# Optimization experiments

Measured on AMD Instinct MI355X. Metric: run time of the kernel, lower is better.

## Reference

```python
import jax, jax.numpy as jnp
import numpy as np

B, L, C, H = 8, 1024, 1024, 16  # batch, seq_len, n_embed, n_head


def setup_inputs() -> dict:
    key = jax.random.key(0)
    k0, k1, k2 = jax.random.split(key, 3)
    s = 0.02  # init scale
    return {
        "x": jax.random.normal(k0, (B, L, C), jnp.float32),
        "W_qkv": jax.random.normal(k1, (C, 3 * C), jnp.float32) * s,  # (in, out) layout
        "b_qkv": jnp.zeros((3 * C,), jnp.float32),
        "W_proj": jax.random.normal(k2, (C, C), jnp.float32) * s,
        "b_proj": jnp.zeros((C,), jnp.float32),
    }


def reference(x, W_qkv, b_qkv, W_proj, b_proj):
    Bb, Ll, Cc = x.shape
    d = Cc // H  # head dim
    qkv = x @ W_qkv + b_qkv                      # (B, L, 3C)
    q, k, v = jnp.split(qkv, 3, axis=2)
    q = q.reshape(Bb, Ll, H, d).transpose(0, 2, 1, 3)  # (B, H, L, d)
    k = k.reshape(Bb, Ll, H, d).transpose(0, 2, 1, 3)
    v = v.reshape(Bb, Ll, H, d).transpose(0, 2, 1, 3)
    scale = 1.0 / np.sqrt(d).astype(np.float32)
    attn = jnp.einsum("bhid,bhjd->bhij", q, k) * scale  # (B, H, Lq, Lk)
    causal = jnp.tril(jnp.ones((Ll, Ll), dtype=bool))    # (Lq, Lk)
    attn = jnp.where(causal[None, None, :, :], attn, -jnp.inf)
    # NOTE: source uses F.softmax(attn, dim=2) -> softmax over the QUERY axis.
    attn = jax.nn.softmax(attn, axis=2)
    y = jnp.einsum("bhij,bhjd->bhid", attn, v)           # (B, H, L, d)
    y = y.transpose(0, 2, 1, 3).reshape(Bb, Ll, Cc)      # (B, L, C)
    return y @ W_proj + b_proj
```

## Files before the change

kernel.cpp:

```cpp
#include <hip/hip_runtime.h>

typedef unsigned short u16;
typedef unsigned int   u32;
using bf16x8 = __attribute__((ext_vector_type(8))) short;
using f32x4  = __attribute__((ext_vector_type(4))) float;
using f32x16 = __attribute__((ext_vector_type(16))) float;
using u32x4  = __attribute__((ext_vector_type(4))) u32;

static constexpr int Bb = 8, Ll = 1024, Cc = 1024, Hh = 16, Dd = 64;
static constexpr int Mrows = Bb * Ll;
static constexpr int N3    = 3 * Cc;
static constexpr float QSCALE = 0.125f * 1.44269504088896f;

__device__ __forceinline__ u16 f2b(float f) {
    u32 u = __builtin_bit_cast(u32, f);
    u += 0x7FFFu + ((u >> 16) & 1u);
    return (u16)(u >> 16);
}
__device__ __forceinline__ float b2f(u16 u) {
    return __builtin_bit_cast(float, (u32)u << 16);
}
__device__ __forceinline__ u32 pack2bf(float a, float b) {
    return (u32)f2b(a) | ((u32)f2b(b) << 16);
}
__device__ __forceinline__ void gload16(const u16* g, u16* l) {
    __builtin_amdgcn_global_load_lds(
        (const __attribute__((address_space(1))) void*)g,
        (__attribute__((address_space(3))) void*)l, 16, 0, 0);
}

__global__ void k_f32_to_bf16(const float* __restrict__ in, u16* __restrict__ out, int n16) {
    int idx = blockIdx.x * blockDim.x + threadIdx.x;
    if (idx >= n16) return;
    #pragma unroll
    for (int h = 0; h < 2; ++h) {
        f32x4 v0 = *((const f32x4*)in + idx * 4 + h * 2);
        f32x4 v1 = *((const f32x4*)in + idx * 4 + h * 2 + 1);
        u32x4 o;
        o[0] = pack2bf(v0[0], v0[1]);
        o[1] = pack2bf(v0[2], v0[3]);
        o[2] = pack2bf(v1[0], v1[1]);
        o[3] = pack2bf(v1[2], v1[3]);
        *((u32x4*)out + idx * 2 + h) = o;
    }
}

__global__ void k_transpose_w(const float* __restrict__ Wqkv, u16* __restrict__ WqkvT,
                              const float* __restrict__ Wproj, u16* __restrict__ WprojT) {
    __shared__ float tile[32][33];
    int bx = blockIdx.x;
    const float* in; u16* out; int Cn;
    if (bx < 96) { in = Wqkv;  out = WqkvT;  Cn = N3; }
    else         { in = Wproj; out = WprojT; Cn = Cc; bx -= 96; }
    const int R = Cc;
    int tx = threadIdx.x, ty = threadIdx.y;
    int c = bx * 32 + tx;
    int rbase = blockIdx.y * 32;
    #pragma unroll
    for (int rr = 0; rr < 4; ++rr)
        tile[ty + rr * 8][tx] = in[(size_t)(rbase + ty + rr * 8) * Cn + c];
    __syncthreads();
    int ro = bx * 32 + ty;
    #pragma unroll
    for (int rr = 0; rr < 4; ++rr)
        out[(size_t)(ro + rr * 8) * R + rbase + tx] = f2b(tile[tx][ty + rr * 8]);
}

__global__ void k_transpose_scale_bf16(const u16* __restrict__ in, const float* __restrict__ zinv,
                                       u16* __restrict__ out, int R, int Cn) {
    __shared__ u16 tile[32][33];
    int bh = blockIdx.z;
    size_t base = (size_t)bh * R * Cn;
    int tx = threadIdx.x, ty = threadIdx.y;
    int c = blockIdx.x * 32 + tx;
    int rbase = blockIdx.y * 32;
    #pragma unroll
    for (int rr = 0; rr < 4; ++rr)
        tile[ty + rr * 8][tx] = in[base + (size_t)(rbase + ty + rr * 8) * Cn + c];
    __syncthreads();
    float zv = zinv[(size_t)bh * R + rbase + tx];
    int ro = blockIdx.x * 32 + ty;
    #pragma unroll
    for (int rr = 0; rr < 4; ++rr)
        out[base + (size_t)(ro + rr * 8) * R + rbase + tx] = f2b(b2f(tile[tx][ty + rr * 8]) * zv);
}

__global__ __launch_bounds__(256, 2)
void k_gemm_qkv32(const u16* __restrict__ A, const u16* __restrict__ Bt,
                  const float* __restrict__ bias,
                  u16* __restrict__ qo, u16* __restrict__ ko, u16* __restrict__ vo)
{
    const int K = Cc;
    const int NT = K / 64;
    __shared__ u16 As[2][128 * 64];
    __shared__ u16 Bs[2][128 * 64];
    const int tid = threadIdx.x;
    const int wid = tid >> 6, lane = tid & 63;
    const int l31 = lane & 31, lhi = lane >> 5, l7 = lane & 7;
    const int wr = wid >> 1, wc = wid & 1;
    const int nwg = gridDim.x * gridDim.y;
    const int flat = blockIdx.y * gridDim.x + blockIdx.x;
    const int swz = (flat & 7) * (nwg >> 3) + (flat >> 3);
    const int bx = swz % gridDim.x, by = swz / gridDim.x;
    const int row0 = by * 128, col0 = bx * 128;

    const int srow = tid >> 3;
    const int schunk = (tid & 7) ^ (srow & 7);
    const u16* gA = A  + (size_t)(row0 + srow) * K + schunk * 8;
    const u16* gB = Bt + (size_t)(col0 + srow) * K + schunk * 8;

#define STG(buf, t) do { \
    const u16* ga_ = gA + (size_t)(t) * 64; \
    const u16* gb_ = gB + (size_t)(t) * 64; \
    u16* la_ = &As[buf][wid * 512]; \
    u16* lb_ = &Bs[buf][wid * 512]; \
    gload16(ga_,                  la_); \
    gload16(ga_ + (size_t)32 * K, la_ + 2048); \
    gload16(ga_ + (size_t)64 * K, la_ + 4096); \
    gload16(ga_ + (size_t)96 * K, la_ + 6144); \
    gload16(gb_,                  lb_); \
    gload16(gb_ + (size_t)32 * K, lb_ + 2048); \
    gload16(gb_ + (size_t)64 * K, lb_ + 4096); \
    gload16(gb_ + (size_t)96 * K, lb_ + 6144); \
} while (0)

    const int coff0 = (((0 + lhi) ^ l7) << 3);
    const int coff1 = (((2 + lhi) ^ l7) << 3);
    const int coff2 = (((4 + lhi) ^ l7) << 3);
    const int coff3 = (((6 + lhi) ^ l7) << 3);
    const int coff[4] = { coff0, coff1, coff2, coff3 };

    f32x16 acc[2][2] = {};

    STG(0, 0);
    STG(1, 1);
    asm volatile("s_waitcnt vmcnt(8)" ::: "memory");
    __builtin_amdgcn_s_barrier();
    __builtin_amdgcn_sched_barrier(0);

    for (int t = 0; t < NT; ++t) {
        const u16* cA = &As[t & 1][0];
        const u16* cB = &Bs[t & 1][0];
        bf16x8 af[2][4], bf0[4];
        #pragma unroll
        for (int tm = 0; tm < 2; ++tm)
            #pragma unroll
            for (int kc = 0; kc < 4; ++kc)
                af[tm][kc] = *(const bf16x8*)&cA[(wr * 64 + tm * 32 + l31) * 64 + coff[kc]];
        #pragma unroll
        for (int kc = 0; kc < 4; ++kc)
            bf0[kc] = *(const bf16x8*)&cB[(wc * 64 + l31) * 64 + coff[kc]];
        __builtin_amdgcn_s_setprio(1);
        #pragma unroll
        for (int tm = 0; tm < 2; ++tm)
            #pragma unroll
            for (int kc = 0; kc < 4; ++kc)
                acc[tm][0] = __builtin_amdgcn_mfma_f32_32x32x16_bf16(
                    af[tm][kc], bf0[kc], acc[tm][0], 0, 0, 0);
        __builtin_amdgcn_s_setprio(0);
        __builtin_amdgcn_s_barrier();
        bf16x8 bf1[4];
        #pragma unroll
        for (int kc = 0; kc < 4; ++kc)
            bf1[kc] = *(const bf16x8*)&cB[(wc * 64 + 32 + l31) * 64 + coff[kc]];
        __builtin_amdgcn_s_setprio(1);
        #pragma unroll
        for (int tm = 0; tm < 2; ++tm)
            #pragma unroll
            for (int kc = 0; kc < 4; ++kc)
                acc[tm][1] = __builtin_amdgcn_mfma_f32_32x32x16_bf16(
                    af[tm][kc], bf1[kc], acc[tm][1], 0, 0, 0);
        __builtin_amdgcn_s_setprio(0);
        __builtin_amdgcn_s_barrier();
        __builtin_amdgcn_sched_barrier(0);
        if (t + 2 < NT) STG(t & 1, t + 2);
        if (t + 1 < NT) {
            if (t + 2 < NT) { asm volatile("s_waitcnt vmcnt(8)" ::: "memory"); }
            else            { asm volatile("s_waitcnt vmcnt(0)" ::: "memory"); }
            __builtin_amdgcn_s_barrier();
            __builtin_amdgcn_sched_barrier(0);
        }
    }
#undef STG

    #pragma unroll
    for (int tm = 0; tm < 2; ++tm) {
        #pragma unroll
        for (int tn = 0; tn < 2; ++tn) {
            int cg = col0 + wc * 64 + tn * 32 + l31;
            float bv = bias[cg];
            int which = cg >> 10;
            float sc = (which == 0) ? QSCALE : 1.0f;
            int cc2 = cg & 1023;
            int h = cc2 >> 6, dd = cc2 & 63;
            int rbase = row0 + wr * 64 + tm * 32 + 4 * lhi;
            #pragma unroll
            for (int g = 0; g < 4; ++g) {
                #pragma unroll
                for (int r = 0; r < 4; ++r) {
                    int rg = rbase + 8 * g + r;
                    int bidx = rg >> 10, ll2 = rg & 1023;
                    size_t o = ((size_t)(bidx * Hh + h) * Ll + ll2) * Dd + dd;
                    u16 val = f2b((acc[tm][tn][g * 4 + r] + bv) * sc);
                    if (which == 0) qo[o] = val;
                    else if (which == 1) ko[o] = val;
                    else vo[o] = val;
                }
            }
        }
    }
}

__global__ __launch_bounds__(256, 2)
void k_gemm_proj32(const u16* __restrict__ A, const u16* __restrict__ Bt,
                   const float* __restrict__ bias, float* __restrict__ outf)
{
    const int K = Cc;
    const int N = Cc;
    const int NT = K / 64;
    __shared__ u16 As[2][128 * 64];
    __shared__ u16 Bs[2][128 * 64];
    const int tid = threadIdx.x;
    const int wid = tid >> 6, lane = tid & 63;
    const int l31 = lane & 31, lhi = lane >> 5, l7 = lane & 7;
    const int wr = wid >> 1, wc = wid & 1;
    const int nwg = gridDim.x * gridDim.y;
    const int flat = blockIdx.y * gridDim.x + blockIdx.x;
    const int swz = (flat & 7) * (nwg >> 3) + (flat >> 3);
    const int bx = swz % gridDim.x, by = swz / gridDim.x;
    const int row0 = by * 128, col0 = bx * 128;

    const int srow = tid >> 3;
    const int schunk = (tid & 7) ^ (srow & 7);
    const u16* gA = A  + (size_t)(row0 + srow) * K + schunk * 8;
    const u16* gB = Bt + (size_t)(col0 + srow) * K + schunk * 8;

#define STG(buf, t) do { \
    const u16* ga_ = gA + (size_t)(t) * 64; \
    const u16* gb_ = gB + (size_t)(t) * 64; \
    u16* la_ = &As[buf][wid * 512]; \
    u16* lb_ = &Bs[buf][wid * 512]; \
    gload16(ga_,                  la_); \
    gload16(ga_ + (size_t)32 * K, la_ + 2048); \
    gload16(ga_ + (size_t)64 * K, la_ + 4096); \
    gload16(ga_ + (size_t)96 * K, la_ + 6144); \
    gload16(gb_,                  lb_); \
    gload16(gb_ + (size_t)32 * K, lb_ + 2048); \
    gload16(gb_ + (size_t)64 * K, lb_ + 4096); \
    gload16(gb_ + (size_t)96 * K, lb_ + 6144); \
} while (0)

    const int coff0 = (((0 + lhi) ^ l7) << 3);
    const int coff1 = (((2 + lhi) ^ l7) << 3);
    const int coff2 = (((4 + lhi) ^ l7) << 3);
    const int coff3 = (((6 + lhi) ^ l7) << 3);
    const int coff[4] = { coff0, coff1, coff2, coff3 };

    f32x16 acc[2][2] = {};

    STG(0, 0);
    STG(1, 1);
    asm volatile("s_waitcnt vmcnt(8)" ::: "memory");
    __builtin_amdgcn_s_barrier();
    __builtin_amdgcn_sched_barrier(0);

    for (int t = 0; t < NT; ++t) {
        const u16* cA = &As[t & 1][0];
        const u16* cB = &Bs[t & 1][0];
        bf16x8 af[2][4], bf0[4];
        #pragma unroll
        for (int tm = 0; tm < 2; ++tm)
            #pragma unroll
            for (int kc = 0; kc < 4; ++kc)
                af[tm][kc] = *(const bf16x8*)&cA[(wr * 64 + tm * 32 + l31) * 64 + coff[kc]];
        #pragma unroll
        for (int kc = 0; kc < 4; ++kc)
            bf0[kc] = *(const bf16x8*)&cB[(wc * 64 + l31) * 64 + coff[kc]];
        __builtin_amdgcn_s_setprio(1);
        #pragma unroll
        for (int tm = 0; tm < 2; ++tm)
            #pragma unroll
            for (int kc = 0; kc < 4; ++kc)
                acc[tm][0] = __builtin_amdgcn_mfma_f32_32x32x16_bf16(
                    af[tm][kc], bf0[kc], acc[tm][0], 0, 0, 0);
        __builtin_amdgcn_s_setprio(0);
        __builtin_amdgcn_s_barrier();
        bf16x8 bf1[4];
        #pragma unroll
        for (int kc = 0; kc < 4; ++kc)
            bf1[kc] = *(const bf16x8*)&cB[(wc * 64 + 32 + l31) * 64 + coff[kc]];
        __builtin_amdgcn_s_setprio(1);
        #pragma unroll
        for (int tm = 0; tm < 2; ++tm)
            #pragma unroll
            for (int kc = 0; kc < 4; ++kc)
                acc[tm][1] = __builtin_amdgcn_mfma_f32_32x32x16_bf16(
                    af[tm][kc], bf1[kc], acc[tm][1], 0, 0, 0);
        __builtin_amdgcn_s_setprio(0);
        __builtin_amdgcn_s_barrier();
        __builtin_amdgcn_sched_barrier(0);
        if (t + 2 < NT) STG(t & 1, t + 2);
        if (t + 1 < NT) {
            if (t + 2 < NT) { asm volatile("s_waitcnt vmcnt(8)" ::: "memory"); }
            else            { asm volatile("s_waitcnt vmcnt(0)" ::: "memory"); }
            __builtin_amdgcn_s_barrier();
            __builtin_amdgcn_sched_barrier(0);
        }
    }
#undef STG

    #pragma unroll
    for (int tm = 0; tm < 2; ++tm) {
        #pragma unroll
        for (int tn = 0; tn < 2; ++tn) {
            int cg = col0 + wc * 64 + tn * 32 + l31;
            float bv = bias[cg];
            int rbase = row0 + wr * 64 + tm * 32 + 4 * lhi;
            #pragma unroll
            for (int g = 0; g < 4; ++g) {
                #pragma unroll
                for (int r = 0; r < 4; ++r) {
                    int rg = rbase + 8 * g + r;
                    outf[(size_t)rg * N + cg] = acc[tm][tn][g * 4 + r] + bv;
                }
            }
        }
    }
}

__global__ __launch_bounds__(256, 4)
void k_attn_colsum(const u16* __restrict__ Q, const u16* __restrict__ Kb,
                   float* __restrict__ zinv)
{
    __shared__ u16 Qs[2][64 * 64];
    const int tid = threadIdx.x;
    const int wid = tid >> 6, lane = tid & 63;
    const int lr = lane & 15, lg = lane >> 4;
    const int l7 = lr & 7;
    const int fid = blockIdx.x;
    const int xcd = fid & 7, n = fid >> 3;
    const int xtA = n & 7;
    const int xtB = 15 - xtA;
    const int bh = (xcd << 4) | (n >> 3);
    const u16* Qp = Q  + (size_t)bh * Ll * Dd;
    const u16* Kp = Kb + (size_t)bh * Ll * Dd;
    const int jwA = xtA * 64 + wid * 16;
    const int jwB = xtB * 64 + wid * 16;
    bf16x8 kbA0 = *(const bf16x8*)&Kp[(jwA + lr) * Dd + lg * 8];
    bf16x8 kbA1 = *(const bf16x8*)&Kp[(jwA + lr) * Dd + 32 + lg * 8];
    bf16x8 kbB0 = *(const bf16x8*)&Kp[(jwB + lr) * Dd + lg * 8];
    bf16x8 kbB1 = *(const bf16x8*)&Kp[(jwB + lr) * Dd + 32 + lg * 8];
    const bool dmask[4] = { lg * 4 + 0 >= lr, lg * 4 + 1 >= lr,
                            lg * 4 + 2 >= lr, lg * 4 + 3 >= lr };
    const int ch0 = ((lg ^ l7) << 3);
    const int ch1 = (((4 + lg) ^ l7) << 3);
    const int srow = tid >> 3;
    const int schunk = (tid & 7) ^ (srow & 7);
    float zA = 0.f, zB = 0.f;

    const int nA = 16 - xtA;
    const int NS = 17;
#define IOF(s) (((s) < nA) ? (xtA * 64 + 64 * (s)) : (xtB * 64 + 64 * ((s) - nA)))

#define STGQ(buf, I0) do { \
    const u16* g_ = Qp + (size_t)((I0) + srow) * 64 + schunk * 8; \
    u16* l_ = &Qs[buf][wid * 512]; \
    gload16(g_,                   l_); \
    gload16(g_ + (size_t)32 * 64, l_ + 2048); \
} while (0)

#define CS_STEP(buf, I0, JW, KB0, KB1, ZACC) do { \
    const u16* Qs_ = &Qs[buf][0]; \
    _Pragma("unroll") \
    for (int ss = 0; ss < 4; ++ss) { \
        int ib = (I0) + ss * 16; \
        if (ib >= (JW)) { \
            bf16x8 qa0 = *(const bf16x8*)&Qs_[(ss * 16 + lr) * 64 + ch0]; \
            bf16x8 qa1 = *(const bf16x8*)&Qs_[(ss * 16 + lr) * 64 + ch1]; \
            f32x4 s_ = {0.f, 0.f, 0.f, 0.f}; \
            s_ = __builtin_amdgcn_mfma_f32_16x16x32_bf16(qa0, KB0, s_, 0, 0, 0); \
            s_ = __builtin_amdgcn_mfma_f32_16x16x32_bf16(qa1, KB1, s_, 0, 0, 0); \
            if (ib >= (JW) + 16) { \
                _Pragma("unroll") \
                for (int r = 0; r < 4; ++r) ZACC += exp2f(s_[r]); \
            } else { \
                _Pragma("unroll") \
                for (int r = 0; r < 4; ++r) ZACC += dmask[r] ? exp2f(s_[r]) : 0.f; \
            } \
        } \
    } \
} while (0)

    STGQ(0, IOF(0));
    STGQ(1, IOF(1));
    asm volatile("s_waitcnt vmcnt(2)" ::: "memory");
    __builtin_amdgcn_s_barrier();
    __builtin_amdgcn_sched_barrier(0);

    for (int s = 0; s < NS; ++s) {
        if (s < nA) { CS_STEP((s & 1), xtA * 64 + 64 * s, jwA, kbA0, kbA1, zA); }
        else        { CS_STEP((s & 1), xtB * 64 + 64 * (s - nA), jwB, kbB0, kbB1, zB); }
        __builtin_amdgcn_s_barrier();
        __builtin_amdgcn_sched_barrier(0);
        if (s + 2 < NS) STGQ((s & 1), IOF(s + 2));
        if (s + 1 < NS) {
            if (s + 2 < NS) { asm volatile("s_waitcnt vmcnt(2)" ::: "memory"); }
            else            { asm volatile("s_waitcnt vmcnt(0)" ::: "memory"); }
            __builtin_amdgcn_s_barrier();
            __builtin_amdgcn_sched_barrier(0);
        }
    }
#undef STGQ
#undef CS_STEP
#undef IOF

    zA += __shfl_xor(zA, 16); zA += __shfl_xor(zA, 32);
    zB += __shfl_xor(zB, 16); zB += __shfl_xor(zB, 32);
    if (lg == 0) {
        zinv[(size_t)bh * Ll + jwA + lr] = 1.f / zA;
        zinv[(size_t)bh * Ll + jwB + lr] = 1.f / zB;
    }
}

__global__ __launch_bounds__(256, 4)
void k_attn_pv(const u16* __restrict__ Q, const u16* __restrict__ Kb,
               const u16* __restrict__ Vt, u16* __restrict__ Y)
{
    __shared__ u16 Ks[2][64 * 64];
    __shared__ u16 Vs[2][64 * 64];
    const int tid = threadIdx.x;
    const int wid = tid >> 6, lane = tid & 63;
    const int lr = lane & 15, lg = lane >> 4;
    const int l7 = lr & 7;
    const int fid = blockIdx.x;
    const int xcd = fid & 7, n = fid >> 3;
    const int xtA = n & 7;
    const int xtB = 15 - xtA;
    const int bh = (xcd << 4) | (n >> 3);
    const int bidx = bh >> 4, h = bh & 15;
    const u16* Qp = Q  + (size_t)bh * Ll * Dd;
    const u16* Kp = Kb + (size_t)bh * Ll * Dd;
    const u16* Vp = Vt + (size_t)bh * Ll * Dd;
    const int src0 = lr + 32 * (lg & 1);
    const int src1 = src0 + 16;
    const bool selHi = (lg & 2) != 0;
    const int ch0 = ((lg ^ l7) << 3);
    const int ch1 = (((4 + lg) ^ l7) << 3);
    const int srow = tid >> 3;
    const int schunk = (tid & 7) ^ (srow & 7);

    const int iwA = xtA * 64 + wid * 16;
    const int iwB = xtB * 64 + wid * 16;
    bf16x8 qaA0 = *(const bf16x8*)&Qp[(iwA + lr) * Dd + lg * 8];
    bf16x8 qaA1 = *(const bf16x8*)&Qp[(iwA + lr) * Dd + 32 + lg * 8];
    bf16x8 qaB0 = *(const bf16x8*)&Qp[(iwB + lr) * Dd + lg * 8];
    bf16x8 qaB1 = *(const bf16x8*)&Qp[(iwB + lr) * Dd + 32 + lg * 8];
    f32x4 yaccA[4] = {};
    f32x4 yaccB[4] = {};

    const int NS = 17;
#define JOF(s) (((s) <= xtA) ? 64 * (s) : 64 * ((s) - xtA - 1))

#define STGKV(buf, J) do { \
    const u16* gk_ = Kp + (size_t)((J) + srow) * 64 + schunk * 8; \
    const u16* gv_ = Vp + (size_t)srow * Ll + (J) + schunk * 8; \
    u16* lk_ = &Ks[buf][wid * 512]; \
    u16* lv_ = &Vs[buf][wid * 512]; \
    gload16(gk_,                   lk_); \
    gload16(gk_ + (size_t)32 * 64, lk_ + 2048); \
    gload16(gv_,                   lv_); \
    gload16(gv_ + (size_t)32 * Ll, lv_ + 2048); \
} while (0)

#define PV_STEP(buf, J0, IW, QA0, QA1, YACC) do { \
    const u16* Ks_ = &Ks[buf][0]; \
    const u16* Vs_ = &Vs[buf][0]; \
    uint2 w0, w1, w2, w3; \
    _Pragma("unroll") \
    for (int cs = 0; cs < 4; ++cs) { \
        bf16x8 kb0 = *(const bf16x8*)&Ks_[(cs * 16 + lr) * 64 + ch0]; \
        bf16x8 kb1 = *(const bf16x8*)&Ks_[(cs * 16 + lr) * 64 + ch1]; \
        f32x4 s_ = {0.f, 0.f, 0.f, 0.f}; \
        s_ = __builtin_amdgcn_mfma_f32_16x16x32_bf16(kb0, QA0, s_, 0, 0, 0); \
        s_ = __builtin_amdgcn_mfma_f32_16x16x32_bf16(kb1, QA1, s_, 0, 0, 0); \
        int jb = (J0) + cs * 16; \
        float p[4]; \
        if (jb + 15 <= (IW)) { \
            _Pragma("unroll") \
            for (int r = 0; r < 4; ++r) p[r] = exp2f(s_[r]); \
        } else { \
            int ig = (IW) + lr; \
            _Pragma("unroll") \
            for (int r = 0; r < 4; ++r) \
                p[r] = (jb + 4 * lg + r <= ig) ? exp2f(s_[r]) : 0.f; \
        } \
        uint2 w_; \
        w_.x = pack2bf(p[0], p[1]); \
        w_.y = pack2bf(p[2], p[3]); \
        if (cs == 0) w0 = w_; else if (cs == 1) w1 = w_; \
        else if (cs == 2) w2 = w_; else w3 = w_; \
    } \
    u32 a00 = (u32)__shfl((int)w0.x, src0), a01 = (u32)__shfl((int)w0.y, src0); \
    u32 a02 = (u32)__shfl((int)w0.x, src1), a03 = (u32)__shfl((int)w0.y, src1); \
    u32 a10 = (u32)__shfl((int)w1.x, src0), a11 = (u32)__shfl((int)w1.y, src0); \
    u32 a12 = (u32)__shfl((int)w1.x, src1), a13 = (u32)__shfl((int)w1.y, src1); \
    u32 a20 = (u32)__shfl((int)w2.x, src0), a21 = (u32)__shfl((int)w2.y, src0); \
    u32 a22 = (u32)__shfl((int)w2.x, src1), a23 = (u32)__shfl((int)w2.y, src1); \
    u32 a30 = (u32)__shfl((int)w3.x, src0), a31 = (u32)__shfl((int)w3.y, src0); \
    u32 a32 = (u32)__shfl((int)w3.x, src1), a33 = (u32)__shfl((int)w3.y, src1); \
    u32x4 pa0u, pa1u; \
    pa0u[0] = selHi ? a10 : a00;  pa0u[1] = selHi ? a11 : a01; \
    pa0u[2] = selHi ? a12 : a02;  pa0u[3] = selHi ? a13 : a03; \
    pa1u[0] = selHi ? a30 : a20;  pa1u[1] = selHi ? a31 : a21; \
    pa1u[2] = selHi ? a32 : a22;  pa1u[3] = selHi ? a33 : a23; \
    bf16x8 pa0 = __builtin_bit_cast(bf16x8, pa0u); \
    bf16x8 pa1 = __builtin_bit_cast(bf16x8, pa1u); \
    _Pragma("unroll") \
    for (int ns = 0; ns < 4; ++ns) { \
        bf16x8 vb0 = *(const bf16x8*)&Vs_[(ns * 16 + lr) * 64 + ch0]; \
        bf16x8 vb1 = *(const bf16x8*)&Vs_[(ns * 16 + lr) * 64 + ch1]; \
        YACC[ns] = __builtin_amdgcn_mfma_f32_16x16x32_bf16(pa0, vb0, YACC[ns], 0, 0, 0); \
        YACC[ns] = __builtin_amdgcn_mfma_f32_16x16x32_bf16(pa1, vb1, YACC[ns], 0, 0, 0); \
    } \
} while (0)

    STGKV(0, 0);
    STGKV(1, JOF(1));
    asm volatile("s_waitcnt vmcnt(4)" ::: "memory");
    __builtin_amdgcn_s_barrier();
    __builtin_amdgcn_sched_barrier(0);

    for (int s = 0; s < NS; ++s) {
        if (s <= xtA) { PV_STEP((s & 1), 64 * s, iwA, qaA0, qaA1, yaccA); }
        else          { PV_STEP((s & 1), 64 * (s - xtA - 1), iwB, qaB0, qaB1, yaccB); }
        __builtin_amdgcn_s_barrier();
        __builtin_amdgcn_sched_barrier(0);
        if (s + 2 < NS) STGKV((s & 1), JOF(s + 2));
        if (s + 1 < NS) {
            if (s + 2 < NS) { asm volatile("s_waitcnt vmcnt(4)" ::: "memory"); }
            else            { asm volatile("s_waitcnt vmcnt(0)" ::: "memory"); }
            __builtin_amdgcn_s_barrier();
            __builtin_amdgcn_sched_barrier(0);
        }
    }
#undef STGKV
#undef PV_STEP
#undef JOF

    #pragma unroll
    for (int ns = 0; ns < 4; ++ns)
        #pragma unroll
        for (int r = 0; r < 4; ++r) {
            int l2 = iwA + lg * 4 + r;
            Y[((size_t)bidx * Ll + l2) * Cc + h * Dd + ns * 16 + lr] = f2b(yaccA[ns][r]);
        }
    #pragma unroll
    for (int ns = 0; ns < 4; ++ns)
        #pragma unroll
        for (int r = 0; r < 4; ++r) {
            int l2 = iwB + lg * 4 + r;
            Y[((size_t)bidx * Ll + l2) * Cc + h * Dd + ns * 16 + lr] = f2b(yaccB[ns][r]);
        }
}

extern "C" void kernel_launch(void* const* d_in, const int* in_sizes, int n_in,
                              void* d_out, int out_size, void* d_ws, size_t ws_size,
                              hipStream_t stream)
{
    const float* x     = (const float*)d_in[0];
    const float* Wqkv  = (const float*)d_in[1];
    const float* bqkv  = (const float*)d_in[2];
    const float* Wproj = (const float*)d_in[3];
    const float* bproj = (const float*)d_in[4];
    float* out = (float*)d_out;

    char* ws = (char*)d_ws;
    u16* xb     = (u16*)(ws + 0);
    u16* WqkvT  = (u16*)(ws + 16777216);
    u16* WprojT = (u16*)(ws + 23068672);
    u16* q      = (u16*)(ws + 25165824);
    u16* k      = (u16*)(ws + 41943040);
    u16* v      = (u16*)(ws + 58720256);
    u16* vt     = (u16*)(ws + 75497472);
    float* zinv = (float*)(ws + 92274688);

    k_f32_to_bf16<<<dim3(2048), dim3(256), 0, stream>>>(x, xb, Mrows * Cc / 16);
    k_transpose_w<<<dim3(128, 32), dim3(32, 8), 0, stream>>>(Wqkv, WqkvT, Wproj, WprojT);
    k_gemm_qkv32<<<dim3(N3 / 128, Mrows / 128), dim3(256), 0, stream>>>(
        xb, WqkvT, bqkv, q, k, v);
    k_attn_colsum<<<dim3(1024), dim3(256), 0, stream>>>(q, k, zinv);
    k_transpose_scale_bf16<<<dim3(2, 32, Bb * Hh), dim3(32, 8), 0, stream>>>(v, zinv, vt, Ll, Dd);
    k_attn_pv<<<dim3(1024), dim3(256), 0, stream>>>(q, k, vt, v);
    k_gemm_proj32<<<dim3(Cc / 128, Mrows / 128), dim3(256), 0, stream>>>(
        v, WprojT, bproj, out);
}
```

Measured before the change: 183.9 us.

## Fuse prep kernels and fold V transpose-scale into colsum kernel

Merges the x-to-bf16 conversion and the weight transpose into one launch. It also moves the V transpose and the 1/z column scaling into the tail of the column-sum attention kernel, using LDS to stage the V tile and the z inverses. This drops two kernel launches and the global round trip for zinv, so the workspace for zinv is no longer needed. In exchange, the colsum kernel does extra tail work with added barriers, and its LDS transpose reads may hit bank conflicts.

```diff
diff --git a/kernel.cpp b/kernel.cpp
--- a/kernel.cpp
+++ b/kernel.cpp
@@ -29,33 +29,38 @@
         (__attribute__((address_space(3))) void*)l, 16, 0, 0);
 }
 
-__global__ void k_f32_to_bf16(const float* __restrict__ in, u16* __restrict__ out, int n16) {
-    int idx = blockIdx.x * blockDim.x + threadIdx.x;
-    if (idx >= n16) return;
-    #pragma unroll
-    for (int h = 0; h < 2; ++h) {
-        f32x4 v0 = *((const f32x4*)in + idx * 4 + h * 2);
-        f32x4 v1 = *((const f32x4*)in + idx * 4 + h * 2 + 1);
-        u32x4 o;
-        o[0] = pack2bf(v0[0], v0[1]);
-        o[1] = pack2bf(v0[2], v0[3]);
-        o[2] = pack2bf(v1[0], v1[1]);
-        o[3] = pack2bf(v1[2], v1[3]);
-        *((u32x4*)out + idx * 2 + h) = o;
-    }
-}
-
-__global__ void k_transpose_w(const float* __restrict__ Wqkv, u16* __restrict__ WqkvT,
-                              const float* __restrict__ Wproj, u16* __restrict__ WprojT) {
+__global__ void k_prep(const float* __restrict__ x, u16* __restrict__ xb,
+                       const float* __restrict__ Wqkv, u16* __restrict__ WqkvT,
+                       const float* __restrict__ Wproj, u16* __restrict__ WprojT)
+{
     __shared__ float tile[32][33];
-    int bx = blockIdx.x;
+    int bid = blockIdx.x;
+    int tid = threadIdx.x;
+    if (bid < 2048) {
+        int idx = bid * 256 + tid;
+        #pragma unroll
+        for (int h = 0; h < 2; ++h) {
+            f32x4 v0 = *((const f32x4*)x + idx * 4 + h * 2);
+            f32x4 v1 = *((const f32x4*)x + idx * 4 + h * 2 + 1);
+            u32x4 o;
+            o[0] = pack2bf(v0[0], v0[1]);
+            o[1] = pack2bf(v0[2], v0[3]);
+            o[2] = pack2bf(v1[0], v1[1]);
+            o[3] = pack2bf(v1[2], v1[3]);
+            *((u32x4*)xb + idx * 2 + h) = o;
+        }
+        return;
+    }
+    int bz = bid - 2048;
+    int bx = bz & 127;
+    int by = bz >> 7;
     const float* in; u16* out; int Cn;
     if (bx < 96) { in = Wqkv;  out = WqkvT;  Cn = N3; }
     else         { in = Wproj; out = WprojT; Cn = Cc; bx -= 96; }
     const int R = Cc;
-    int tx = threadIdx.x, ty = threadIdx.y;
+    int tx = tid & 31, ty = tid >> 5;
     int c = bx * 32 + tx;
-    int rbase = blockIdx.y * 32;
+    int rbase = by * 32;
     #pragma unroll
     for (int rr = 0; rr < 4; ++rr)
         tile[ty + rr * 8][tx] = in[(size_t)(rbase + ty + rr * 8) * Cn + c];
@@ -64,25 +69,6 @@
     #pragma unroll
     for (int rr = 0; rr < 4; ++rr)
         out[(size_t)(ro + rr * 8) * R + rbase + tx] = f2b(tile[tx][ty + rr * 8]);
-}
-
-__global__ void k_transpose_scale_bf16(const u16* __restrict__ in, const float* __restrict__ zinv,
-                                       u16* __restrict__ out, int R, int Cn) {
-    __shared__ u16 tile[32][33];
-    int bh = blockIdx.z;
-    size_t base = (size_t)bh * R * Cn;
-    int tx = threadIdx.x, ty = threadIdx.y;
-    int c = blockIdx.x * 32 + tx;
-    int rbase = blockIdx.y * 32;
-    #pragma unroll
-    for (int rr = 0; rr < 4; ++rr)
-        tile[ty + rr * 8][tx] = in[base + (size_t)(rbase + ty + rr * 8) * Cn + c];
-    __syncthreads();
-    float zv = zinv[(size_t)bh * R + rbase + tx];
-    int ro = blockIdx.x * 32 + ty;
-    #pragma unroll
-    for (int rr = 0; rr < 4; ++rr)
-        out[base + (size_t)(ro + rr * 8) * R + rbase + tx] = f2b(b2f(tile[tx][ty + rr * 8]) * zv);
 }
 
 __global__ __launch_bounds__(256, 2)
@@ -329,10 +315,11 @@
 }
 
 __global__ __launch_bounds__(256, 4)
-void k_attn_colsum(const u16* __restrict__ Q, const u16* __restrict__ Kb,
-                   float* __restrict__ zinv)
+void k_attn_colsum_vt(const u16* __restrict__ Q, const u16* __restrict__ Kb,
+                      const u16* __restrict__ V, u16* __restrict__ vt)
 {
     __shared__ u16 Qs[2][64 * 64];
+    __shared__ float zlds[2][64];
     const int tid = threadIdx.x;
     const int wid = tid >> 6, lane = tid & 63;
     const int lr = lane & 15, lg = lane >> 4;
@@ -417,8 +404,32 @@
     zA += __shfl_xor(zA, 16); zA += __shfl_xor(zA, 32);
     zB += __shfl_xor(zB, 16); zB += __shfl_xor(zB, 32);
     if (lg == 0) {
-        zinv[(size_t)bh * Ll + jwA + lr] = 1.f / zA;
-        zinv[(size_t)bh * Ll + jwB + lr] = 1.f / zB;
+        zlds[0][wid * 16 + lr] = 1.f / zA;
+        zlds[1][wid * 16 + lr] = 1.f / zB;
+    }
+
+    u16* sc = &Qs[0][0];
+    const u16* Vr = V + (size_t)bh * Ll * Dd;
+    const int lrow = tid >> 2;
+    const int seg  = (tid & 3) << 4;
+    #pragma unroll
+    for (int t = 0; t < 2; ++t) {
+        const int jw0 = (t ? xtB : xtA) * 64;
+        u32x4 h0 = *(const u32x4*)&Vr[(size_t)(jw0 + lrow) * Dd + seg];
+        u32x4 h1 = *(const u32x4*)&Vr[(size_t)(jw0 + lrow) * Dd + seg + 8];
+        __syncthreads();
+        *(u32x4*)&sc[lrow * 72 + seg]     = h0;
+        *(u32x4*)&sc[lrow * 72 + seg + 8] = h1;
+        __syncthreads();
+        u16 obuf[16];
+        #pragma unroll
+        for (int j = 0; j < 16; ++j) {
+            float zv = zlds[t][seg + j];
+            obuf[j] = f2b(b2f(sc[(seg + j) * 72 + lrow]) * zv);
+        }
+        u16* dst = vt + ((size_t)bh * Dd + lrow) * Ll + jw0 + seg;
+        *(u32x4*)dst       = *(u32x4*)&obuf[0];
+        *(u32x4*)(dst + 8) = *(u32x4*)&obuf[8];
     }
 }
 
@@ -582,14 +593,11 @@
     u16* k      = (u16*)(ws + 41943040);
     u16* v      = (u16*)(ws + 58720256);
     u16* vt     = (u16*)(ws + 75497472);
-    float* zinv = (float*)(ws + 92274688);
-
-    k_f32_to_bf16<<<dim3(2048), dim3(256), 0, stream>>>(x, xb, Mrows * Cc / 16);
-    k_transpose_w<<<dim3(128, 32), dim3(32, 8), 0, stream>>>(Wqkv, WqkvT, Wproj, WprojT);
+
+    k_prep<<<dim3(2048 + 4096), dim3(256), 0, stream>>>(x, xb, Wqkv, WqkvT, Wproj, WprojT);
     k_gemm_qkv32<<<dim3(N3 / 128, Mrows / 128), dim3(256), 0, stream>>>(
         xb, WqkvT, bqkv, q, k, v);
-    k_attn_colsum<<<dim3(1024), dim3(256), 0, stream>>>(q, k, zinv);
-    k_transpose_scale_bf16<<<dim3(2, 32, Bb * Hh), dim3(32, 8), 0, stream>>>(v, zinv, vt, Ll, Dd);
+    k_attn_colsum_vt<<<dim3(1024), dim3(256), 0, stream>>>(q, k, v, vt);
     k_attn_pv<<<dim3(1024), dim3(256), 0, stream>>>(q, k, vt, v);
     k_gemm_proj32<<<dim3(Cc / 128, Mrows / 128), dim3(256), 0, stream>>>(
         v, WprojT, bproj, out);
```

Measured after the change: 175.0 us, median of 3. 1.05x faster.
